# Optimization experiments

Hardware: AMD Instinct MI355X
Metric: run time of the kernel (lower is better)

The kernel has to match this reference:

```python
import jax, jax.numpy as jnp
import numpy as np
from jax import lax

EPS = 1e-5
K = 32  # k_neighbor

def conv1(x, w):
    # x: [B, Cin, L], w: [Cout, Cin] (1x1 conv, no bias)
    return jnp.einsum('bcl,oc->bol', x, w)

def bn(x, g, b):
    # BatchNorm1d in training mode: batch statistics over (batch, length)
    m = jnp.mean(x, axis=(0, 2), keepdims=True)
    v = jnp.var(x, axis=(0, 2), keepdims=True)
    return g[None, :, None] * (x - m) / jnp.sqrt(v + EPS) + b[None, :, None]

def res_block(x, w1, g1, b1, w2, g2, b2):
    h = jax.nn.gelu(bn(conv1(x, w1), g1, b1), approximate=False)
    h = bn(conv1(h, w2), g2, b2)
    return jax.nn.gelu(h + x, approximate=False)

def extraction(x, conv_w, bn_g, bn_b, fw, fg, fb):
    # conv_w: [n_blocks, 2, C, C]; bn_g/bn_b: [n_blocks, 2, C]
    for i in range(conv_w.shape[0]):
        x = res_block(x, conv_w[i, 0], bn_g[i, 0], bn_b[i, 0],
                      conv_w[i, 1], bn_g[i, 1], bn_b[i, 1])
    # TransformerBlock: ffn (conv+BN) with residual + GELU
    return jax.nn.gelu(x + bn(conv1(x, fw), fg, fb), approximate=False)

def setup_inputs() -> dict:
    key = jax.random.key(0)
    ks = jax.random.split(key, 16)
    B, N, S, C = 8, 4096, 1024, 128  # C = out_channel = 2*channel
    inp = {
        'xyz': jax.random.normal(ks[0], (B, N, 3), dtype=jnp.float32),
        'x': jax.random.normal(ks[1], (B, 64, N), dtype=jnp.float32),
        'fps_idx': jax.random.randint(ks[2], (B, S), 0, N, dtype=jnp.int64),
        'pre_conv_w': jax.random.normal(ks[3], (2, 2, C, C), dtype=jnp.float32) * 0.05,
        'pre_bn_g': jnp.ones((2, 2, C), jnp.float32),
        'pre_bn_b': jnp.zeros((2, 2, C), jnp.float32),
        'pre_ffn_w': jax.random.normal(ks[4], (C, C), dtype=jnp.float32) * 0.05,
        'pre_ffn_g': jnp.ones((C,), jnp.float32),
        'pre_ffn_b': jnp.zeros((C,), jnp.float32),
        'pos_conv_w': jax.random.normal(ks[5], (2, 2, C, C), dtype=jnp.float32) * 0.05,
        'pos_bn_g': jnp.ones((2, 2, C), jnp.float32),
        'pos_bn_b': jnp.zeros((2, 2, C), jnp.float32),
        'pos_ffn_w': jax.random.normal(ks[6], (C, C), dtype=jnp.float32) * 0.05,
        'pos_ffn_g': jnp.ones((C,), jnp.float32),
        'pos_ffn_b': jnp.zeros((C,), jnp.float32),
    }
    return inp

def reference(xyz, x, fps_idx,
              pre_conv_w, pre_bn_g, pre_bn_b, pre_ffn_w, pre_ffn_g, pre_ffn_b,
              pos_conv_w, pos_bn_g, pos_bn_b, pos_ffn_w, pos_ffn_g, pos_ffn_b):
    B, N, _ = xyz.shape
    S = fps_idx.shape[1]
    points = jnp.swapaxes(x, 1, 2)  # [B, N, d]
    d = points.shape[-1]

    # --- LocalGrouper ---
    new_xyz = jnp.take_along_axis(xyz, fps_idx[:, :, None], axis=1)      # [B, S, 3]
    new_pts = jnp.take_along_axis(points, fps_idx[:, :, None], axis=1)  # [B, S, d]

    # squared distances [B, S, N]
    sqr = (jnp.sum(new_xyz ** 2, -1)[:, :, None]
           + jnp.sum(xyz ** 2, -1)[:, None, :]
           - 2.0 * jnp.einsum('bsc,bnc->bsn', new_xyz, xyz))
    idx = lax.top_k(-sqr, K)[1]  # [B, S, K] smallest distances

    grouped = jnp.take_along_axis(points, idx.reshape(B, S * K)[:, :, None],
                                  axis=1).reshape(B, S, K, d)
    center = new_pts[:, :, None, :]  # [B, S, 1, d]
    feat = jnp.concatenate([grouped - center,
                            jnp.broadcast_to(center, grouped.shape)], axis=-1)  # [B,S,K,2d]

    C = 2 * d
    # --- PreExtraction: [B,S,K,C] -> [B*S, C, K] -> maxpool -> [B, C, S] ---
    y = jnp.swapaxes(feat, 2, 3).reshape(B * S, C, K)
    y = extraction(y, pre_conv_w, pre_bn_g, pre_bn_b, pre_ffn_w, pre_ffn_g, pre_ffn_b)
    y = jnp.max(y, axis=-1).reshape(B, S, C)
    y = jnp.swapaxes(y, 1, 2)  # [B, C, S]

    # --- PosExtraction ---
    y = extraction(y, pos_conv_w, pos_bn_g, pos_bn_b, pos_ffn_w, pos_ffn_g, pos_ffn_b)
    return (new_xyz, y)
```

## Files before the change

kernel.cpp:

```cpp
#include <hip/hip_runtime.h>
#include <math.h>

typedef unsigned short ushort_t;
typedef unsigned long long u64;
typedef unsigned int uint32;

#define B_ 8
#define N_ 4096
#define S_ 1024
#define K_ 32
#define C_ 128
#define NCOL1 (B_*S_*K_)
#define NCOL2 (B_*S_)
#define EPS_ 1e-5f

typedef ushort_t us8 __attribute__((ext_vector_type(8)));
typedef short s16x8 __attribute__((ext_vector_type(8)));
typedef float f32x4 __attribute__((ext_vector_type(4)));

__device__ __forceinline__ float bf2f(ushort_t u){ return __uint_as_float(((uint32)u)<<16); }
__device__ __forceinline__ ushort_t f2bf(float f){
    uint32 x = __float_as_uint(f);
    return (ushort_t)((x + 0x7FFFu + ((x>>16)&1u)) >> 16);
}
__device__ __forceinline__ float gelu_f(float v){
    float az = fabsf(v)*0.70710678118654752f;
    float t  = __builtin_amdgcn_rcpf(fmaf(0.3275911f, az, 1.0f));
    float p  = fmaf(fmaf(fmaf(fmaf(1.061405429f, t, -1.453152027f), t, 1.421413741f), t,
                   -0.284496736f), t, 0.254829592f)*t;
    float e  = __expf(-az*az);
    float er = fmaf(-p, e, 1.0f);
    float s  = (v < 0.0f) ? -er : er;
    return 0.5f*v*(1.0f+s);
}
__device__ __forceinline__ u64 shfl_xor_u64(u64 v, int m){
    int lo = __shfl_xor((int)(v & 0xFFFFFFFFull), m, 64);
    int hi = __shfl_xor((int)(v >> 32), m, 64);
    return (((u64)(uint32)hi) << 32) | (uint32)lo;
}
__device__ __forceinline__ void gl_lds16(const char* gp, char* lp){
    __builtin_amdgcn_global_load_lds((const __attribute__((address_space(1))) void*)gp,
                                     (__attribute__((address_space(3))) void*)lp, 16, 0, 0);
}

__global__ __launch_bounds__(256) void transpose_kernel(const float* __restrict__ x, ushort_t* __restrict__ xTb){
    __shared__ float t[64][65];
    int b  = blockIdx.x >> 6;
    int n0 = (blockIdx.x & 63) * 64;
    int tx = threadIdx.x & 63, ty = threadIdx.x >> 6;
    #pragma unroll
    for (int i=0;i<16;i++){
        int c = i*4 + ty;
        t[c][tx] = x[((long)(b*64 + c))*N_ + n0 + tx];
    }
    __syncthreads();
    #pragma unroll
    for (int i=0;i<16;i++){
        int n = i*4 + ty;
        xTb[((long)(b*N_ + n0 + n))*64 + tx] = f2bf(t[tx][n]);
    }
}

__global__ __launch_bounds__(256) void knn_kernel(const float* __restrict__ xyz, const int* __restrict__ fps,
                                                  int* __restrict__ idxg, float* __restrict__ newxyz){
    __shared__ uint32 hist[4096];
    __shared__ u64    cand[1024];
    __shared__ u64    out_keys[64];
    __shared__ uint32 csum[256];
    __shared__ uint32 wtot[4];
    __shared__ uint32 shv[8];
    __shared__ u64    wred[4];
    __shared__ u64    winner;

    int tid = threadIdx.x;
    int wv = tid >> 6, l = tid & 63;
    int bs = blockIdx.x;
    int b  = bs >> 10;
    int qi = fps[bs];
    const float* qb = xyz + ((long)b*N_ + qi)*3;
    float qx = qb[0], qy = qb[1], qz = qb[2];
    if (tid < 3) newxyz[(long)bs*3 + tid] = qb[tid];
    const float* xb = xyz + (long)b*N_*3;

    for (int i=tid;i<1024;i+=256) hist[i]=0;
    if (tid < 8) shv[tid]=0;
    __syncthreads();

    uint32 dbits[16];
    #pragma unroll
    for (int i=0;i<16;i++){
        int n = i*256 + tid;
        float dx = xb[n*3+0]-qx, dy = xb[n*3+1]-qy, dz = xb[n*3+2]-qz;
        float d = dx*dx + dy*dy + dz*dz;
        dbits[i] = __float_as_uint(d);
        atomicAdd(&hist[dbits[i]>>21], 1u);
    }
    __syncthreads();

    {
        uint32 h4[4]; uint32 csumv=0;
        #pragma unroll
        for (int i=0;i<4;i++){ h4[i]=hist[tid*4+i]; csumv+=h4[i]; }
        uint32 sc = csumv;
        #pragma unroll
        for (int off=1; off<64; off<<=1){ uint32 o=__shfl_up(sc,off,64); if (l>=off) sc+=o; }
        if (l==63) wtot[wv]=sc;
        csum[tid]=sc;
        __syncthreads();
        uint32 base=0;
        for (int w2=0; w2<wv; w2++) base += wtot[w2];
        uint32 cum = base + csum[tid] - csumv;
        #pragma unroll
        for (int i=0;i<4;i++){
            if (cum <= 31u && 31u < cum + h4[i]){ shv[0]=(uint32)(tid*4+i); shv[1]=cum; }
            cum += h4[i];
        }
    }
    __syncthreads();
    uint32 b1 = shv[0], cl1 = shv[1];

    for (int i=tid;i<4096;i+=256) hist[i]=0;
    __syncthreads();
    #pragma unroll
    for (int i=0;i<16;i++){
        uint32 u = dbits[i];
        if ((u>>21)==b1) atomicAdd(&hist[(u>>9)&0xFFFu], 1u);
    }
    __syncthreads();

    uint32 r2 = 31u - cl1;
    {
        uint32 h[16]; uint32 csumv=0;
        #pragma unroll
        for (int i=0;i<16;i++){ h[i]=hist[tid*16+i]; csumv += h[i]; }
        uint32 sc = csumv;
        #pragma unroll
        for (int off=1; off<64; off<<=1){ uint32 o=__shfl_up(sc,off,64); if (l>=off) sc+=o; }
        if (l==63) wtot[wv]=sc;
        csum[tid]=sc;
        __syncthreads();
        uint32 base=0;
        for (int w2=0; w2<wv; w2++) base += wtot[w2];
        uint32 cum = base + csum[tid] - csumv;
        #pragma unroll
        for (int i=0;i<16;i++){
            if (cum <= r2 && r2 < cum + h[i]){ shv[2]=(uint32)(tid*16+i); shv[3]=cum; }
            cum += h[i];
        }
    }
    __syncthreads();
    uint32 b2 = shv[2], cl2 = shv[3];
    uint32 nless = cl1 + cl2;

    #pragma unroll
    for (int i=0;i<16;i++){
        uint32 u = dbits[i];
        int n = i*256 + tid;
        uint32 bb1 = u >> 21;
        if (bb1 > b1) continue;
        u64 key = (((u64)u)<<32) | (uint32)n;
        if (bb1 < b1){
            uint32 p = atomicAdd(&shv[4],1u); out_keys[p] = key;
        } else {
            uint32 bb2 = (u>>9)&0xFFFu;
            if (bb2 < b2){ uint32 p = atomicAdd(&shv[4],1u); out_keys[p] = key; }
            else if (bb2 == b2){ uint32 p = atomicAdd(&shv[5],1u); if (p < 1024u) cand[p] = key; }
        }
    }
    __syncthreads();

    if (shv[5] > 1024u){
        uint32 alive = 0xFFFFu;
        for (int r=0;r<K_;r++){
            u64 lmin = ~0ull;
            #pragma unroll
            for (int i=0;i<16;i++){
                u64 k = (((u64)dbits[i])<<32) | (uint32)(i*256+tid);
                if (((alive>>i)&1u) && k < lmin) lmin = k;
            }
            #pragma unroll
            for (int off=32; off>=1; off>>=1){
                u64 o = shfl_xor_u64(lmin, off);
                if (o < lmin) lmin = o;
            }
            if (l == 0) wred[wv] = lmin;
            __syncthreads();
            if (tid == 0){
                u64 m = wred[0];
                if (wred[1]<m) m=wred[1];
                if (wred[2]<m) m=wred[2];
                if (wred[3]<m) m=wred[3];
                winner = m;
                idxg[(long)bs*K_ + r] = (int)(m & 0xFFFFFFFFull);
            }
            __syncthreads();
            u64 w = winner;
            #pragma unroll
            for (int i=0;i<16;i++){
                u64 k = (((u64)dbits[i])<<32) | (uint32)(i*256+tid);
                if (k == w) alive &= ~(1u<<i);
            }
        }
    } else if (wv == 0){
        uint32 cb   = shv[5];
        uint32 need = 32u - nless;
        for (uint32 r=0; r<need; r++){
            u64 lmin = ~0ull;
            for (uint32 s=l; s<cb; s+=64){ u64 kk = cand[s]; if (kk < lmin) lmin = kk; }
            #pragma unroll
            for (int off=32; off>=1; off>>=1){
                u64 o = shfl_xor_u64(lmin, off);
                if (o < lmin) lmin = o;
            }
            for (uint32 s=l; s<cb; s+=64){ if (cand[s]==lmin) cand[s] = ~0ull; }
            if (l==0) out_keys[nless + r] = lmin;
        }
        u64 key = (l < 32) ? out_keys[l] : ~0ull;
        #pragma unroll
        for (uint32 k=2; k<=64; k<<=1){
            bool dir = ((l & k)==0);
            #pragma unroll
            for (uint32 j=k>>1; j>=1; j>>=1){
                u64 o = shfl_xor_u64(key, j);
                bool lower = ((l & j)==0);
                u64 mn = (key < o) ? key : o;
                u64 mx = (key < o) ? o : key;
                key = (lower == dir) ? mn : mx;
            }
        }
        if (l < 32) idxg[(long)bs*K_ + l] = (int)(key & 0xFFFFFFFFull);
    }
}

__global__ __launch_bounds__(256) void wcvt_kernel(const float* __restrict__ pcw, const float* __restrict__ pfw,
                                                   const float* __restrict__ qcw, const float* __restrict__ qfw,
                                                   ushort_t* __restrict__ Wb, ushort_t* __restrict__ UW,
                                                   ushort_t* __restrict__ VW){
    int i = blockIdx.x*256 + threadIdx.x;
    if (i < 163840){
        int mat = i >> 14;
        int r = i & 16383;
        float v;
        if (mat < 4)       v = pcw[i];
        else if (mat == 4) v = pfw[r];
        else if (mat < 9)  v = qcw[i - 5*16384];
        else               v = qfw[r];
        Wb[i] = f2bf(v);
    } else {
        int j = i - 163840;
        int jj = j & 8191;
        int oc = jj >> 6, c = jj & 63;
        if (j < 8192) UW[jj] = f2bf(pcw[oc*128 + c]);
        else          VW[jj] = f2bf(pcw[oc*128 + 64 + c] - pcw[oc*128 + c]);
    }
}

__global__ __launch_bounds__(256) void uv_gemm(const ushort_t* __restrict__ xTb, const int* __restrict__ fps,
                                               const ushort_t* __restrict__ UW, const ushort_t* __restrict__ VW,
                                               ushort_t* __restrict__ U, ushort_t* __restrict__ V2){
    int tid = threadIdx.x;
    int w = tid >> 6, l = tid & 63;
    int l15 = l & 15, l4 = l >> 4;
    bool isV = blockIdx.x >= 256;
    int base = (isV ? (int)(blockIdx.x - 256) : (int)blockIdx.x)*128 + w*32;
    const ushort_t* Wh = isV ? VW : UW;
    ushort_t* out = isV ? V2 : U;

    long xrow[2];
    #pragma unroll
    for (int n=0;n<2;n++){
        int r = base + n*16 + l15;
        if (isV){ int b = r >> 10; xrow[n] = ((long)(b<<12) + fps[r]); }
        else    { xrow[n] = r; }
    }
    f32x4 acc[8][2] = {};
    #pragma unroll
    for (int ks=0; ks<2; ks++){
        int kl = ks*32 + l4*8;
        s16x8 af[8];
        #pragma unroll
        for (int m=0;m<8;m++)
            af[m] = *(const s16x8*)(Wh + (m*16 + l15)*64 + kl);
        s16x8 bv[2];
        #pragma unroll
        for (int n=0;n<2;n++)
            bv[n] = *(const s16x8*)(xTb + xrow[n]*64 + kl);
        #pragma unroll
        for (int m=0;m<8;m++)
            #pragma unroll
            for (int n=0;n<2;n++)
                acc[m][n] = __builtin_amdgcn_mfma_f32_16x16x32_bf16(af[m], bv[n], acc[m][n], 0, 0, 0);
    }
    #pragma unroll
    for (int n=0;n<2;n++){
        long radr = (long)(base + n*16 + l15)*C_;
        #pragma unroll
        for (int m=0;m<8;m++){
            f32x4 a = acc[m][n];
            uint2 st;
            st.x = (((uint32)f2bf(a[1]))<<16) | f2bf(a[0]);
            st.y = (((uint32)f2bf(a[3]))<<16) | f2bf(a[2]);
            *(uint2*)(out + radr + m*16 + l4*4) = st;
        }
    }
}

template<int MODE>
__global__ __launch_bounds__(256) void conv_mfma(const ushort_t* in1, const ushort_t* in2, ushort_t* aux,
                                                 ushort_t* out, const ushort_t* __restrict__ Wb,
                                                 const float* __restrict__ scsh_g,
                                                 const ushort_t* __restrict__ U, const ushort_t* __restrict__ V2,
                                                 const ushort_t* __restrict__ xTb, const int* __restrict__ idxg,
                                                 const int* __restrict__ fps,
                                                 float* __restrict__ pb, int nb, float inv_cnt){
    __shared__ ushort_t inT[16384];
    __shared__ float ss[256];
    __shared__ float sL[4][128], qL[4][128];
    int tid = threadIdx.x;
    int w = tid >> 6, l = tid & 63;
    int l15 = l & 15, l4 = l >> 4;
    long col0 = ((long)blockIdx.x << 7) + ((long)w << 5);

    if (MODE != 3){
        const char* gt = (const char*)(in1 + (((long)blockIdx.x) << 7)*C_);
        char* lb = (char*)inT;
        #pragma unroll
        for (int i=0;i<8;i++){
            int p = i*4096 + w*1024 + l*16;
            int src = p ^ (((p>>8)&7)<<4);
            gl_lds16(gt + src, lb + i*4096 + w*1024);
        }
    }

    s16x8 a2[8];
    if (MODE == 2){
        #pragma unroll
        for (int t=0;t<8;t++){
            int n = t>>2, ks = t&3;
            a2[t] = *(const s16x8*)(in2 + (col0 + n*16 + l15)*C_ + ks*32 + l4*8);
        }
    }
    if (MODE == 4){
        int bs = (int)(col0 >> 5);
        int b  = bs >> 10;
        int cc = fps[bs];
        const ushort_t* crow = xTb + ((long)(b<<12) + cc)*64;
        s16x8 c0 = *(const s16x8*)(crow + l4*8);
        s16x8 c1 = *(const s16x8*)(crow + 32 + l4*8);
        #pragma unroll
        for (int n=0;n<2;n++){
            int nn = idxg[col0 + n*16 + l15];
            const ushort_t* prow = xTb + ((long)(b<<12) + nn)*64;
            s16x8 p0 = *(const s16x8*)(prow + l4*8);
            s16x8 p1 = *(const s16x8*)(prow + 32 + l4*8);
            s16x8 d0, d1;
            #pragma unroll
            for (int e=0;e<8;e++){
                d0[e] = (short)f2bf(bf2f((ushort_t)p0[e]) - bf2f((ushort_t)c0[e]));
                d1[e] = (short)f2bf(bf2f((ushort_t)p1[e]) - bf2f((ushort_t)c1[e]));
            }
            a2[n*4+0] = d0; a2[n*4+1] = d1; a2[n*4+2] = c0; a2[n*4+3] = c1;
        }
    }
    if (MODE == 1 || MODE == 2 || MODE == 4) ss[tid] = scsh_g[tid];
    __syncthreads();

    f32x4 acc[8][2] = {};
    if (MODE == 3){
        int bs = (int)(col0 >> 5);
        int b  = bs >> 10;
        const ushort_t* vrow = V2 + (long)bs*C_;
        #pragma unroll
        for (int n=0;n<2;n++){
            int nn = idxg[col0 + n*16 + l15];
            const ushort_t* urow = U + ((long)(b*4096) + nn)*C_;
            #pragma unroll
            for (int m=0;m<8;m++){
                int oc0 = m*16 + l4*4;
                uint2 uu = *(const uint2*)(urow + oc0);
                uint2 vv = *(const uint2*)(vrow + oc0);
                acc[m][n][0] = bf2f((ushort_t)(uu.x & 0xFFFFu)) + bf2f((ushort_t)(vv.x & 0xFFFFu));
                acc[m][n][1] = bf2f((ushort_t)(uu.x >> 16))     + bf2f((ushort_t)(vv.x >> 16));
                acc[m][n][2] = bf2f((ushort_t)(uu.y & 0xFFFFu)) + bf2f((ushort_t)(vv.y & 0xFFFFu));
                acc[m][n][3] = bf2f((ushort_t)(uu.y >> 16))     + bf2f((ushort_t)(vv.y >> 16));
            }
        }
    } else {
        char* lb = (char*)inT;
        #pragma unroll
        for (int ks=0; ks<4; ks++){
            int kl = ks*32 + l4*8;
            s16x8 af[8];
            #pragma unroll
            for (int m=0;m<8;m++)
                af[m] = *(const s16x8*)(Wb + (m*16 + l15)*C_ + kl);
            s16x8 bv[2];
            int qsv[2];
            #pragma unroll
            for (int n=0;n<2;n++){
                int q = (w*32 + n*16 + l15)*256 + ks*64 + l4*16;
                qsv[n] = q ^ (((q>>8)&7)<<4);
                bv[n] = *(const s16x8*)(lb + qsv[n]);
            }
            if (MODE != 0){
                float sc[8], sh[8];
                const float4* sp = (const float4*)(&ss[kl*2]);
                float4 s0 = sp[0], s1 = sp[1], s2 = sp[2], s3 = sp[3];
                sc[0]=s0.x; sh[0]=s0.y; sc[1]=s0.z; sh[1]=s0.w;
                sc[2]=s1.x; sh[2]=s1.y; sc[3]=s1.z; sh[3]=s1.w;
                sc[4]=s2.x; sh[4]=s2.y; sc[5]=s2.z; sh[5]=s2.w;
                sc[6]=s3.x; sh[6]=s3.y; sc[7]=s3.z; sh[7]=s3.w;
                #pragma unroll
                for (int n=0;n<2;n++){
                    s16x8 v = bv[n];
                    if (MODE == 1){
                        #pragma unroll
                        for (int e=0;e<8;e++){
                            float f = gelu_f(fmaf(bf2f((ushort_t)v[e]), sc[e], sh[e]));
                            v[e] = (short)f2bf(f);
                        }
                    } else {
                        s16x8 a = a2[n*4+ks];
                        #pragma unroll
                        for (int e=0;e<8;e++){
                            float f = gelu_f(fmaf(bf2f((ushort_t)v[e]), sc[e], sh[e]) + bf2f((ushort_t)a[e]));
                            v[e] = (short)f2bf(f);
                        }
                    }
                    bv[n] = v;
                    if (MODE == 2 || MODE == 4)
                        *(s16x8*)(lb + qsv[n]) = v;
                }
            }
            #pragma unroll
            for (int m=0;m<8;m++)
                #pragma unroll
                for (int n=0;n<2;n++)
                    acc[m][n] = __builtin_amdgcn_mfma_f32_16x16x32_bf16(af[m], bv[n], acc[m][n], 0, 0, 0);
        }
    }

    if (MODE == 2 || MODE == 4){
        __syncthreads();
        char* auxb = (char*)aux + ((long)blockIdx.x << 15);
        const char* lb = (const char*)inT;
        #pragma unroll
        for (int i=0;i<8;i++){
            int lin = i*4096 + tid*16;
            int qs = lin ^ (((lin>>8)&7)<<4);
            *(f32x4*)(auxb + lin) = *(const f32x4*)(lb + qs);
        }
        __syncthreads();
    }

    {
        char* lb = (char*)inT;
        #pragma unroll
        for (int n=0;n<2;n++){
            #pragma unroll
            for (int m=0;m<8;m++){
                f32x4 a = acc[m][n];
                uint2 st;
                st.x = (((uint32)f2bf(a[1]))<<16) | f2bf(a[0]);
                st.y = (((uint32)f2bf(a[3]))<<16) | f2bf(a[2]);
                int q = (w*32 + n*16 + l15)*256 + (m*16 + l4*4)*2;
                int qs = q ^ (((q>>8)&7)<<4);
                *(uint2*)(lb + qs) = st;
            }
        }
        __syncthreads();
        char* outb = (char*)out + ((long)blockIdx.x << 15);
        const char* lb2 = (const char*)inT;
        #pragma unroll
        for (int i=0;i<8;i++){
            int lin = i*4096 + tid*16;
            int qs = lin ^ (((lin>>8)&7)<<4);
            *(f32x4*)(outb + lin) = *(const f32x4*)(lb2 + qs);
        }
    }

    #pragma unroll
    for (int m=0;m<8;m++){
        #pragma unroll
        for (int r=0;r<4;r++){
            float a0=acc[m][0][r], a1=acc[m][1][r];
            float s = a0+a1;
            float q = a0*a0+a1*a1;
            #pragma unroll
            for (int off=1; off<16; off<<=1){
                s += __shfl_xor(s, off, 64);
                q += __shfl_xor(q, off, 64);
            }
            if (l15 == 0){
                sL[w][m*16 + l4*4 + r] = s;
                qL[w][m*16 + l4*4 + r] = q;
            }
        }
    }
    __syncthreads();
    if (tid < 128){
        float s = sL[0][tid] + sL[1][tid] + sL[2][tid] + sL[3][tid];
        float q = qL[0][tid] + qL[1][tid] + qL[2][tid] + qL[3][tid];
        pb[(long)tid*nb + blockIdx.x]       = s;
        pb[(long)(128+tid)*nb + blockIdx.x] = q;
    }
}

__global__ __launch_bounds__(256) void reduce_fin_kernel(const float* __restrict__ pb, float* __restrict__ scsh,
                                                         const float* __restrict__ g, const float* __restrict__ bb,
                                                         float inv_cnt, int nb){
    int oc = blockIdx.x;
    float s=0.f, q=0.f;
    for (int b=threadIdx.x; b<nb; b+=256){
        s += pb[(long)oc*nb + b];
        q += pb[(long)(128+oc)*nb + b];
    }
    __shared__ float ls[256], lq[256];
    ls[threadIdx.x]=s; lq[threadIdx.x]=q;
    __syncthreads();
    #pragma unroll
    for (int st_=128; st_>0; st_>>=1){
        if (threadIdx.x < st_){ ls[threadIdx.x]+=ls[threadIdx.x+st_]; lq[threadIdx.x]+=lq[threadIdx.x+st_]; }
        __syncthreads();
    }
    if (threadIdx.x==0){
        float mean = ls[0]*inv_cnt;
        float var  = lq[0]*inv_cnt - mean*mean;
        float sc   = g[oc]*rsqrtf(var + EPS_);
        scsh[oc*2+0] = sc;
        scsh[oc*2+1] = bb[oc] - mean*sc;
    }
}

__global__ __launch_bounds__(256) void pool_kernel(const ushort_t* __restrict__ T, const ushort_t* __restrict__ X,
                                                   const float* __restrict__ scsh, ushort_t* __restrict__ A2){
    long p  = (long)blockIdx.x*256 + threadIdx.x;
    long bs = p >> 6;
    int  c0 = ((int)p & 63)*2;
    float sc0=scsh[c0*2], sh0=scsh[c0*2+1], sc1=scsh[c0*2+2], sh1=scsh[c0*2+3];
    const ushort_t* tb = T + (bs*K_)*(long)C_ + c0;
    const ushort_t* xv = X + (bs*K_)*(long)C_ + c0;
    float m0 = -1e30f, m1 = -1e30f;
    #pragma unroll 4
    for (int k=0;k<K_;k++){
        uint32 tv = *(const uint32*)(tb + (long)k*C_);
        uint32 av = *(const uint32*)(xv + (long)k*C_);
        float v0 = gelu_f(fmaf(bf2f((ushort_t)(tv & 0xFFFFu)), sc0, sh0) + bf2f((ushort_t)(av & 0xFFFFu)));
        float v1 = gelu_f(fmaf(bf2f((ushort_t)(tv >> 16)),     sc1, sh1) + bf2f((ushort_t)(av >> 16)));
        m0 = fmaxf(m0, v0);
        m1 = fmaxf(m1, v1);
    }
    uint32 o = (((uint32)f2bf(m1))<<16) | f2bf(m0);
    *(uint32*)(A2 + bs*C_ + c0) = o;
}

__global__ __launch_bounds__(256) void out2_kernel(const ushort_t* __restrict__ T, const ushort_t* __restrict__ X,
                                                   const float* __restrict__ scsh_g, float* __restrict__ y){
    __shared__ ushort_t Ts[16384];
    __shared__ ushort_t Xs[16384];
    __shared__ float ss[256];
    int tid = threadIdx.x, w = tid>>6, l = tid&63;
    int blk = blockIdx.x;

    {
        const char* gt = (const char*)(T + ((long)blk << 7)*C_);
        const char* gx = (const char*)(X + ((long)blk << 7)*C_);
        #pragma unroll
        for (int i=0;i<8;i++){
            int p = i*4096 + w*1024 + l*16;
            int src = p ^ (((p>>8)&7)<<4);
            gl_lds16(gt + src, (char*)Ts + i*4096 + w*1024);
            gl_lds16(gx + src, (char*)Xs + i*4096 + w*1024);
        }
    }
    ss[tid] = scsh_g[tid];
    __syncthreads();

    int b  = blk >> 3;
    int s0 = (blk & 7) * 128;
    int colL = tid & 127;
    int rep  = tid >> 7;
    #pragma unroll
    for (int cb=0; cb<8; cb++){
        int q  = colL*256 + rep*128 + cb*16;
        int qs = q ^ (((q>>8)&7)<<4);
        s16x8 tvv = *(const s16x8*)((char*)Ts + qs);
        s16x8 xvv = *(const s16x8*)((char*)Xs + qs);
        #pragma unroll
        for (int e=0;e<8;e++){
            int c = rep*64 + cb*8 + e;
            float f = gelu_f(fmaf(bf2f((ushort_t)tvv[e]), ss[c*2], ss[c*2+1]) + bf2f((ushort_t)xvv[e]));
            y[((long)(b*C_ + c))*S_ + s0 + colL] = f;
        }
    }
}

extern "C" void kernel_launch(void* const* d_in, const int* in_sizes, int n_in,
                              void* d_out, int out_size, void* d_ws, size_t ws_size,
                              hipStream_t stream){
    const float* xyz        = (const float*)d_in[0];
    const float* x          = (const float*)d_in[1];
    const int*   fps        = (const int*)d_in[2];
    const float* pre_conv_w = (const float*)d_in[3];
    const float* pre_bn_g   = (const float*)d_in[4];
    const float* pre_bn_b   = (const float*)d_in[5];
    const float* pre_ffn_w  = (const float*)d_in[6];
    const float* pre_ffn_g  = (const float*)d_in[7];
    const float* pre_ffn_b  = (const float*)d_in[8];
    const float* pos_conv_w = (const float*)d_in[9];
    const float* pos_bn_g   = (const float*)d_in[10];
    const float* pos_bn_b   = (const float*)d_in[11];
    const float* pos_ffn_w  = (const float*)d_in[12];
    const float* pos_ffn_g  = (const float*)d_in[13];
    const float* pos_ffn_b  = (const float*)d_in[14];

    float* out_xyz = (float*)d_out;
    float* out_y   = (float*)d_out + (long)B_*S_*3;

    char* ws = (char*)d_ws;
    float*    scsh = (float*)(ws + 0);
    float*    pbE  = (float*)(ws + 10240);
    ushort_t* Wb   = (ushort_t*)(ws + 337920);
    ushort_t* UW   = (ushort_t*)(ws + 665600);
    ushort_t* VW   = (ushort_t*)(ws + 681984);
    int*      idx  = (int*)(ws + 698368);
    ushort_t* xTb  = (ushort_t*)(ws + 1746944);
    ushort_t* A2   = (ushort_t*)(ws + 5941248);
    float*    pb1  = (float*)(ws + 8038400);
    ushort_t* C2   = (ushort_t*)(ws + 8038400);
    ushort_t* Cb   = (ushort_t*)(ws + 10135552);
    ushort_t* X    = (ushort_t*)(ws + 77244416);
    ushort_t* U    = (ushort_t*)(ws + 77244416);
    ushort_t* V2   = (ushort_t*)(ws + 85633024);
    (void)in_sizes; (void)n_in; (void)out_size; (void)ws_size;

    const float inv1 = 1.0f/(float)NCOL1, inv2 = 1.0f/(float)NCOL2;
    const ushort_t* Wp = Wb;
    const ushort_t* Wq = Wb + 5*C_*C_;
    const int nb = 2048;

    wcvt_kernel<<<704,256,0,stream>>>(pre_conv_w, pre_ffn_w, pos_conv_w, pos_ffn_w, Wb, UW, VW);
    transpose_kernel<<<B_*(N_/64),256,0,stream>>>(x, xTb);
    knn_kernel<<<B_*S_,256,0,stream>>>(xyz, fps, idx, out_xyz);
    uv_gemm<<<320,256,0,stream>>>(xTb, fps, UW, VW, U, V2);

    {
        const float* G[5]  = {pre_bn_g, pre_bn_g+C_, pre_bn_g+2*C_, pre_bn_g+3*C_, pre_ffn_g};
        const float* Bv[5] = {pre_bn_b, pre_bn_b+C_, pre_bn_b+2*C_, pre_bn_b+3*C_, pre_ffn_b};
        conv_mfma<3><<<nb,256,0,stream>>>(nullptr, nullptr, nullptr, Cb, nullptr, nullptr,
                                          U, V2, nullptr, idx, fps, pb1, nb, inv1);
        reduce_fin_kernel<<<128,256,0,stream>>>(pb1, scsh+0*256, G[0], Bv[0], inv1, nb);
        conv_mfma<1><<<nb,256,0,stream>>>(Cb, nullptr, nullptr, Cb, Wp+1*C_*C_, scsh+0*256,
                                          nullptr, nullptr, nullptr, nullptr, nullptr, pb1, nb, inv1);
        reduce_fin_kernel<<<128,256,0,stream>>>(pb1, scsh+1*256, G[1], Bv[1], inv1, nb);
        conv_mfma<4><<<nb,256,0,stream>>>(Cb, nullptr, X, Cb, Wp+2*C_*C_, scsh+1*256,
                                          nullptr, nullptr, xTb, idx, fps, pb1, nb, inv1);
        reduce_fin_kernel<<<128,256,0,stream>>>(pb1, scsh+2*256, G[2], Bv[2], inv1, nb);
        conv_mfma<1><<<nb,256,0,stream>>>(Cb, nullptr, nullptr, Cb, Wp+3*C_*C_, scsh+2*256,
                                          nullptr, nullptr, nullptr, nullptr, nullptr, pb1, nb, inv1);
        reduce_fin_kernel<<<128,256,0,stream>>>(pb1, scsh+3*256, G[3], Bv[3], inv1, nb);
        conv_mfma<2><<<nb,256,0,stream>>>(Cb, X, X, Cb, Wp+4*C_*C_, scsh+3*256,
                                          nullptr, nullptr, nullptr, nullptr, nullptr, pb1, nb, inv1);
        reduce_fin_kernel<<<128,256,0,stream>>>(pb1, scsh+4*256, G[4], Bv[4], inv1, nb);
        pool_kernel<<<(NCOL2*64)/256,256,0,stream>>>(Cb, X, scsh+4*256, A2);
    }

    {
        const float* G[5]  = {pos_bn_g, pos_bn_g+C_, pos_bn_g+2*C_, pos_bn_g+3*C_, pos_ffn_g};
        const float* Bv[5] = {pos_bn_b, pos_bn_b+C_, pos_bn_b+2*C_, pos_bn_b+3*C_, pos_ffn_b};
        const int nb2 = 64;
        conv_mfma<0><<<nb2,256,0,stream>>>(A2, nullptr, nullptr, C2, Wq+0*C_*C_, nullptr,
                                           nullptr, nullptr, nullptr, nullptr, nullptr, pbE, nb2, inv2);
        reduce_fin_kernel<<<128,256,0,stream>>>(pbE, scsh+5*256, G[0], Bv[0], inv2, nb2);
        conv_mfma<1><<<nb2,256,0,stream>>>(C2, nullptr, nullptr, C2, Wq+1*C_*C_, scsh+5*256,
                                           nullptr, nullptr, nullptr, nullptr, nullptr, pbE, nb2, inv2);
        reduce_fin_kernel<<<128,256,0,stream>>>(pbE, scsh+6*256, G[1], Bv[1], inv2, nb2);
        conv_mfma<2><<<nb2,256,0,stream>>>(C2, A2, A2, C2, Wq+2*C_*C_, scsh+6*256,
                                           nullptr, nullptr, nullptr, nullptr, nullptr, pbE, nb2, inv2);
        reduce_fin_kernel<<<128,256,0,stream>>>(pbE, scsh+7*256, G[2], Bv[2], inv2, nb2);
        conv_mfma<1><<<nb2,256,0,stream>>>(C2, nullptr, nullptr, C2, Wq+3*C_*C_, scsh+7*256,
                                           nullptr, nullptr, nullptr, nullptr, nullptr, pbE, nb2, inv2);
        reduce_fin_kernel<<<128,256,0,stream>>>(pbE, scsh+8*256, G[3], Bv[3], inv2, nb2);
        conv_mfma<2><<<nb2,256,0,stream>>>(C2, A2, A2, C2, Wq+4*C_*C_, scsh+8*256,
                                           nullptr, nullptr, nullptr, nullptr, nullptr, pbE, nb2, inv2);
        reduce_fin_kernel<<<128,256,0,stream>>>(pbE, scsh+9*256, G[4], Bv[4], inv2, nb2);
        out2_kernel<<<64,256,0,stream>>>(C2, A2, scsh+9*256, out_y);
    }
}
```

Before: 583.5 us.

## Fuse BN stat reduction into next conv prologue and store outputs directly

In the small PosExtraction stage, each conv kernel's prologue now reduces the previous layer's 64 per-block partial sums itself and computes the BN scale and shift. This removes four separate reduce_fin launches, and two ping-pong partial buffers avoid read/write hazards. Separately, the conv epilogue and the aux residual store now write straight from registers to global memory instead of staging through swizzled LDS for coalesced stores. That drops syncthreads and an LDS round trip but gives less coalesced 8-byte stores in the large pre-stage kernels.

```diff
diff --git a/kernel.cpp b/kernel.cpp
--- a/kernel.cpp
+++ b/kernel.cpp
@@ -14,7 +14,6 @@
 #define NCOL2 (B_*S_)
 #define EPS_ 1e-5f
 
-typedef ushort_t us8 __attribute__((ext_vector_type(8)));
 typedef short s16x8 __attribute__((ext_vector_type(8)));
 typedef float f32x4 __attribute__((ext_vector_type(4)));
 
@@ -305,14 +304,13 @@
     }
 }
 
-template<int MODE>
+template<int MODE, int PROLOG>
 __global__ __launch_bounds__(256) void conv_mfma(const ushort_t* in1, const ushort_t* in2, ushort_t* aux,
-                                                 ushort_t* out, const ushort_t* __restrict__ Wb,
-                                                 const float* __restrict__ scsh_g,
-                                                 const ushort_t* __restrict__ U, const ushort_t* __restrict__ V2,
-                                                 const ushort_t* __restrict__ xTb, const int* __restrict__ idxg,
-                                                 const int* __restrict__ fps,
-                                                 float* __restrict__ pb, int nb, float inv_cnt){
+        ushort_t* out, const ushort_t* __restrict__ Wb, const float* __restrict__ scsh_g,
+        const ushort_t* __restrict__ U, const ushort_t* __restrict__ V2,
+        const ushort_t* __restrict__ xTb, const int* __restrict__ idxg, const int* __restrict__ fps,
+        const float* __restrict__ pbprev, const float* __restrict__ g, const float* __restrict__ bb,
+        float* __restrict__ pb, int nb, float inv_cnt){
     __shared__ ushort_t inT[16384];
     __shared__ float ss[256];
     __shared__ float sL[4][128], qL[4][128];
@@ -345,8 +343,8 @@
         int b  = bs >> 10;
         int cc = fps[bs];
         const ushort_t* crow = xTb + ((long)(b<<12) + cc)*64;
-        s16x8 c0 = *(const s16x8*)(crow + l4*8);
-        s16x8 c1 = *(const s16x8*)(crow + 32 + l4*8);
+        s16x8 cv0 = *(const s16x8*)(crow + l4*8);
+        s16x8 cv1 = *(const s16x8*)(crow + 32 + l4*8);
         #pragma unroll
         for (int n=0;n<2;n++){
             int nn = idxg[col0 + n*16 + l15];
@@ -356,13 +354,31 @@
             s16x8 d0, d1;
             #pragma unroll
             for (int e=0;e<8;e++){
-                d0[e] = (short)f2bf(bf2f((ushort_t)p0[e]) - bf2f((ushort_t)c0[e]));
-                d1[e] = (short)f2bf(bf2f((ushort_t)p1[e]) - bf2f((ushort_t)c1[e]));
-            }
-            a2[n*4+0] = d0; a2[n*4+1] = d1; a2[n*4+2] = c0; a2[n*4+3] = c1;
-        }
-    }
-    if (MODE == 1 || MODE == 2 || MODE == 4) ss[tid] = scsh_g[tid];
+                d0[e] = (short)f2bf(bf2f((ushort_t)p0[e]) - bf2f((ushort_t)cv0[e]));
+                d1[e] = (short)f2bf(bf2f((ushort_t)p1[e]) - bf2f((ushort_t)cv1[e]));
+            }
+            a2[n*4+0] = d0; a2[n*4+1] = d1; a2[n*4+2] = cv0; a2[n*4+3] = cv1;
+        }
+    }
+    if (MODE == 1 || MODE == 2 || MODE == 4){
+        if (PROLOG){
+            if (tid < 128){
+                const float4* ps = (const float4*)(pbprev + tid*64);
+                const float4* pq = (const float4*)(pbprev + (128+tid)*64);
+                float s=0.f, q=0.f;
+                #pragma unroll
+                for (int i=0;i<16;i++){ float4 a=ps[i]; s += (a.x+a.y)+(a.z+a.w); }
+                #pragma unroll
+                for (int i=0;i<16;i++){ float4 a=pq[i]; q += (a.x+a.y)+(a.z+a.w); }
+                float mean = s*inv_cnt, var = q*inv_cnt - mean*mean;
+                float sc = g[tid]*rsqrtf(var+EPS_);
+                ss[tid*2]   = sc;
+                ss[tid*2+1] = bb[tid] - mean*sc;
+            }
+        } else {
+            ss[tid] = scsh_g[tid];
+        }
+    }
     __syncthreads();
 
     f32x4 acc[8][2] = {};
@@ -386,7 +402,7 @@
             }
         }
     } else {
-        char* lb = (char*)inT;
+        const char* lb = (const char*)inT;
         #pragma unroll
         for (int ks=0; ks<4; ks++){
             int kl = ks*32 + l4*8;
@@ -395,12 +411,11 @@
             for (int m=0;m<8;m++)
                 af[m] = *(const s16x8*)(Wb + (m*16 + l15)*C_ + kl);
             s16x8 bv[2];
-            int qsv[2];
             #pragma unroll
             for (int n=0;n<2;n++){
                 int q = (w*32 + n*16 + l15)*256 + ks*64 + l4*16;
-                qsv[n] = q ^ (((q>>8)&7)<<4);
-                bv[n] = *(const s16x8*)(lb + qsv[n]);
+                int qs = q ^ (((q>>8)&7)<<4);
+                bv[n] = *(const s16x8*)(lb + qs);
             }
             if (MODE != 0){
                 float sc[8], sh[8];
@@ -429,7 +444,7 @@
                     }
                     bv[n] = v;
                     if (MODE == 2 || MODE == 4)
-                        *(s16x8*)(lb + qsv[n]) = v;
+                        *(s16x8*)(aux + (col0 + n*16 + l15)*C_ + kl) = v;
                 }
             }
             #pragma unroll
@@ -440,42 +455,16 @@
         }
     }
 
-    if (MODE == 2 || MODE == 4){
-        __syncthreads();
-        char* auxb = (char*)aux + ((long)blockIdx.x << 15);
-        const char* lb = (const char*)inT;
-        #pragma unroll
-        for (int i=0;i<8;i++){
-            int lin = i*4096 + tid*16;
-            int qs = lin ^ (((lin>>8)&7)<<4);
-            *(f32x4*)(auxb + lin) = *(const f32x4*)(lb + qs);
-        }
-        __syncthreads();
-    }
-
-    {
-        char* lb = (char*)inT;
-        #pragma unroll
-        for (int n=0;n<2;n++){
-            #pragma unroll
-            for (int m=0;m<8;m++){
-                f32x4 a = acc[m][n];
-                uint2 st;
-                st.x = (((uint32)f2bf(a[1]))<<16) | f2bf(a[0]);
-                st.y = (((uint32)f2bf(a[3]))<<16) | f2bf(a[2]);
-                int q = (w*32 + n*16 + l15)*256 + (m*16 + l4*4)*2;
-                int qs = q ^ (((q>>8)&7)<<4);
-                *(uint2*)(lb + qs) = st;
-            }
-        }
-        __syncthreads();
-        char* outb = (char*)out + ((long)blockIdx.x << 15);
-        const char* lb2 = (const char*)inT;
-        #pragma unroll
-        for (int i=0;i<8;i++){
-            int lin = i*4096 + tid*16;
-            int qs = lin ^ (((lin>>8)&7)<<4);
-            *(f32x4*)(outb + lin) = *(const f32x4*)(lb2 + qs);
+    #pragma unroll
+    for (int n=0;n<2;n++){
+        long cadr = (col0 + n*16 + l15)*C_;
+        #pragma unroll
+        for (int m=0;m<8;m++){
+            f32x4 a = acc[m][n];
+            uint2 st;
+            st.x = (((uint32)f2bf(a[1]))<<16) | f2bf(a[0]);
+            st.y = (((uint32)f2bf(a[3]))<<16) | f2bf(a[2]);
+            *(uint2*)(out + cadr + m*16 + l4*4) = st;
         }
     }
 
@@ -601,16 +590,12 @@
     const float* xyz        = (const float*)d_in[0];
     const float* x          = (const float*)d_in[1];
     const int*   fps        = (const int*)d_in[2];
-    const float* pre_conv_w = (const float*)d_in[3];
     const float* pre_bn_g   = (const float*)d_in[4];
     const float* pre_bn_b   = (const float*)d_in[5];
-    const float* pre_ffn_w  = (const float*)d_in[6];
     const float* pre_ffn_g  = (const float*)d_in[7];
     const float* pre_ffn_b  = (const float*)d_in[8];
-    const float* pos_conv_w = (const float*)d_in[9];
     const float* pos_bn_g   = (const float*)d_in[10];
     const float* pos_bn_b   = (const float*)d_in[11];
-    const float* pos_ffn_w  = (const float*)d_in[12];
     const float* pos_ffn_g  = (const float*)d_in[13];
     const float* pos_ffn_b  = (const float*)d_in[14];
 
@@ -619,7 +604,8 @@
 
     char* ws = (char*)d_ws;
     float*    scsh = (float*)(ws + 0);
-    float*    pbE  = (float*)(ws + 10240);
+    float*    pbEa = (float*)(ws + 10240);
+    float*    pbEb = (float*)(ws + 75776);
     ushort_t* Wb   = (ushort_t*)(ws + 337920);
     ushort_t* UW   = (ushort_t*)(ws + 665600);
     ushort_t* VW   = (ushort_t*)(ws + 681984);
@@ -639,7 +625,8 @@
     const ushort_t* Wq = Wb + 5*C_*C_;
     const int nb = 2048;
 
-    wcvt_kernel<<<704,256,0,stream>>>(pre_conv_w, pre_ffn_w, pos_conv_w, pos_ffn_w, Wb, UW, VW);
+    wcvt_kernel<<<704,256,0,stream>>>((const float*)d_in[3], (const float*)d_in[6],
+                                      (const float*)d_in[9], (const float*)d_in[12], Wb, UW, VW);
     transpose_kernel<<<B_*(N_/64),256,0,stream>>>(x, xTb);
     knn_kernel<<<B_*S_,256,0,stream>>>(xyz, fps, idx, out_xyz);
     uv_gemm<<<320,256,0,stream>>>(xTb, fps, UW, VW, U, V2);
@@ -647,20 +634,20 @@
     {
         const float* G[5]  = {pre_bn_g, pre_bn_g+C_, pre_bn_g+2*C_, pre_bn_g+3*C_, pre_ffn_g};
         const float* Bv[5] = {pre_bn_b, pre_bn_b+C_, pre_bn_b+2*C_, pre_bn_b+3*C_, pre_ffn_b};
-        conv_mfma<3><<<nb,256,0,stream>>>(nullptr, nullptr, nullptr, Cb, nullptr, nullptr,
-                                          U, V2, nullptr, idx, fps, pb1, nb, inv1);
+        conv_mfma<3,0><<<nb,256,0,stream>>>(nullptr, nullptr, nullptr, Cb, nullptr, nullptr,
+                                            U, V2, nullptr, idx, fps, nullptr, nullptr, nullptr, pb1, nb, inv1);
         reduce_fin_kernel<<<128,256,0,stream>>>(pb1, scsh+0*256, G[0], Bv[0], inv1, nb);
-        conv_mfma<1><<<nb,256,0,stream>>>(Cb, nullptr, nullptr, Cb, Wp+1*C_*C_, scsh+0*256,
-                                          nullptr, nullptr, nullptr, nullptr, nullptr, pb1, nb, inv1);
+        conv_mfma<1,0><<<nb,256,0,stream>>>(Cb, nullptr, nullptr, Cb, Wp+1*C_*C_, scsh+0*256,
+                                            nullptr, nullptr, nullptr, nullptr, nullptr, nullptr, nullptr, nullptr, pb1, nb, inv1);
         reduce_fin_kernel<<<128,256,0,stream>>>(pb1, scsh+1*256, G[1], Bv[1], inv1, nb);
-        conv_mfma<4><<<nb,256,0,stream>>>(Cb, nullptr, X, Cb, Wp+2*C_*C_, scsh+1*256,
-                                          nullptr, nullptr, xTb, idx, fps, pb1, nb, inv1);
+        conv_mfma<4,0><<<nb,256,0,stream>>>(Cb, nullptr, X, Cb, Wp+2*C_*C_, scsh+1*256,
+                                            nullptr, nullptr, xTb, idx, fps, nullptr, nullptr, nullptr, pb1, nb, inv1);
         reduce_fin_kernel<<<128,256,0,stream>>>(pb1, scsh+2*256, G[2], Bv[2], inv1, nb);
-        conv_mfma<1><<<nb,256,0,stream>>>(Cb, nullptr, nullptr, Cb, Wp+3*C_*C_, scsh+2*256,
-                                          nullptr, nullptr, nullptr, nullptr, nullptr, pb1, nb, inv1);
+        conv_mfma<1,0><<<nb,256,0,stream>>>(Cb, nullptr, nullptr, Cb, Wp+3*C_*C_, scsh+2*256,
+                                            nullptr, nullptr, nullptr, nullptr, nullptr, nullptr, nullptr, nullptr, pb1, nb, inv1);
         reduce_fin_kernel<<<128,256,0,stream>>>(pb1, scsh+3*256, G[3], Bv[3], inv1, nb);
-        conv_mfma<2><<<nb,256,0,stream>>>(Cb, X, X, Cb, Wp+4*C_*C_, scsh+3*256,
-                                          nullptr, nullptr, nullptr, nullptr, nullptr, pb1, nb, inv1);
+        conv_mfma<2,0><<<nb,256,0,stream>>>(Cb, X, X, Cb, Wp+4*C_*C_, scsh+3*256,
+                                            nullptr, nullptr, nullptr, nullptr, nullptr, nullptr, nullptr, nullptr, pb1, nb, inv1);
         reduce_fin_kernel<<<128,256,0,stream>>>(pb1, scsh+4*256, G[4], Bv[4], inv1, nb);
         pool_kernel<<<(NCOL2*64)/256,256,0,stream>>>(Cb, X, scsh+4*256, A2);
     }
@@ -669,21 +656,17 @@
         const float* G[5]  = {pos_bn_g, pos_bn_g+C_, pos_bn_g+2*C_, pos_bn_g+3*C_, pos_ffn_g};
         const float* Bv[5] = {pos_bn_b, pos_bn_b+C_, pos_bn_b+2*C_, pos_bn_b+3*C_, pos_ffn_b};
         const int nb2 = 64;
-        conv_mfma<0><<<nb2,256,0,stream>>>(A2, nullptr, nullptr, C2, Wq+0*C_*C_, nullptr,
-                                           nullptr, nullptr, nullptr, nullptr, nullptr, pbE, nb2, inv2);
-        reduce_fin_kernel<<<128,256,0,stream>>>(pbE, scsh+5*256, G[0], Bv[0], inv2, nb2);
-        conv_mfma<1><<<nb2,256,0,stream>>>(C2, nullptr, nullptr, C2, Wq+1*C_*C_, scsh+5*256,
-                                           nullptr, nullptr, nullptr, nullptr, nullptr, pbE, nb2, inv2);
-        reduce_fin_kernel<<<128,256,0,stream>>>(pbE, scsh+6*256, G[1], Bv[1], inv2, nb2);
-        conv_mfma<2><<<nb2,256,0,stream>>>(C2, A2, A2, C2, Wq+2*C_*C_, scsh+6*256,
-                                           nullptr, nullptr, nullptr, nullptr, nullptr, pbE, nb2, inv2);
-        reduce_fin_kernel<<<128,256,0,stream>>>(pbE, scsh+7*256, G[2], Bv[2], inv2, nb2);
-        conv_mfma<1><<<nb2,256,0,stream>>>(C2, nullptr, nullptr, C2, Wq+3*C_*C_, scsh+7*256,
-                                           nullptr, nullptr, nullptr, nullptr, nullptr, pbE, nb2, inv2);
-        reduce_fin_kernel<<<128,256,0,stream>>>(pbE, scsh+8*256, G[3], Bv[3], inv2, nb2);
-        conv_mfma<2><<<nb2,256,0,stream>>>(C2, A2, A2, C2, Wq+4*C_*C_, scsh+8*256,
-                                           nullptr, nullptr, nullptr, nullptr, nullptr, pbE, nb2, inv2);
-        reduce_fin_kernel<<<128,256,0,stream>>>(pbE, scsh+9*256, G[4], Bv[4], inv2, nb2);
-        out2_kernel<<<64,256,0,stream>>>(C2, A2, scsh+9*256, out_y);
-    }
-}
+        conv_mfma<0,0><<<nb2,256,0,stream>>>(A2, nullptr, nullptr, C2, Wq+0*C_*C_, nullptr,
+                                             nullptr, nullptr, nullptr, nullptr, nullptr, nullptr, nullptr, nullptr, pbEa, nb2, inv2);
+        conv_mfma<1,1><<<nb2,256,0,stream>>>(C2, nullptr, nullptr, C2, Wq+1*C_*C_, nullptr,
+                                             nullptr, nullptr, nullptr, nullptr, nullptr, pbEa, G[0], Bv[0], pbEb, nb2, inv2);
+        conv_mfma<2,1><<<nb2,256,0,stream>>>(C2, A2, A2, C2, Wq+2*C_*C_, nullptr,
+                                             nullptr, nullptr, nullptr, nullptr, nullptr, pbEb, G[1], Bv[1], pbEa, nb2, inv2);
+        conv_mfma<1,1><<<nb2,256,0,stream>>>(C2, nullptr, nullptr, C2, Wq+3*C_*C_, nullptr,
+                                             nullptr, nullptr, nullptr, nullptr, nullptr, pbEa, G[2], Bv[2], pbEb, nb2, inv2);
+        conv_mfma<2,1><<<nb2,256,0,stream>>>(C2, A2, A2, C2, Wq+4*C_*C_, nullptr,
+                                             nullptr, nullptr, nullptr, nullptr, nullptr, pbEb, G[3], Bv[3], pbEa, nb2, inv2);
+        reduce_fin_kernel<<<128,256,0,stream>>>(pbEa, scsh+5*256, G[4], Bv[4], inv2, nb2);
+        out2_kernel<<<64,256,0,stream>>>(C2, A2, scsh+5*256, out_y);
+    }
+}
```

New measurement: 590.0 us. No clear change (+1.1%).
